# Kernel tuning notes

Hardware: AMD Instinct MI355X
Metric: run time of the kernel (lower is better)

The kernel has to match this reference:

```python
import jax, jax.numpy as jnp
import numpy as np

ITERS = 10
SMOOTH = 1e-06


def _pool(x, wh, ww, ph, pw, is_max):
    # torch max_pool2d pads with -inf; min-pool (=-maxpool(-x)) thus pads with +inf.
    init = -jnp.inf if is_max else jnp.inf
    op = jax.lax.max if is_max else jax.lax.min
    return jax.lax.reduce_window(
        x, init, op,
        window_dimensions=(1, 1, wh, ww),
        window_strides=(1, 1, 1, 1),
        padding=((0, 0), (0, 0), (ph, ph), (pw, pw)))


def soft_erode(img):
    p1 = _pool(img, 3, 1, 1, 0, is_max=False)  # min over 3x1 window
    p2 = _pool(img, 1, 3, 0, 1, is_max=False)  # min over 1x3 window
    return jnp.minimum(p1, p2)


def soft_dilate(img):
    return _pool(img, 3, 3, 1, 1, is_max=True)


def soft_open(img):
    return soft_dilate(soft_erode(img))


def soft_skel(img, iters=ITERS):
    skel = jnp.zeros_like(img)
    for _ in range(iters):  # fixed small trip count; unrolled under jit
        opened = soft_open(img)
        skel = skel + jax.nn.relu(img - opened)
        img = soft_erode(img)
    return skel


def setup_inputs() -> dict:
    key = jax.random.key(0)
    k1, k2 = jax.random.split(key)
    B, C, H, W = 16, 1, 512, 512
    pred = jax.random.normal(k1, (B, C, H, W), dtype=jnp.float32)  # logits
    target = jax.random.randint(k2, (B, C, H, W), 0, 2).astype(jnp.float32)
    return {"pred": pred, "target": target}


def reference(pred, target):
    p = jax.nn.sigmoid(pred)
    skel_pred = soft_skel(p, ITERS)
    skel_gt = soft_skel(target.astype(jnp.float32), ITERS)
    tprec = jnp.sum(p * skel_gt) / (jnp.sum(skel_gt) + SMOOTH)
    tsens = jnp.sum(target * skel_pred) / (jnp.sum(skel_pred) + SMOOTH)
    cldice = 2.0 * tprec * tsens / (tprec + tsens + SMOOTH)
    return 1.0 - cldice
```

## Files before the change

kernel.cpp:

```cpp
#include <hip/hip_runtime.h>
#include <math.h>

#define HH 512
#define WW 512
#define NBATCH 16
#define RV 16
#define FSV (HH/RV)
#define FSH 5
#define NF (NBATCH*FSH*FSV)
#define BSU 13
#define BSV 4
#define NBT (NBATCH*BSU*BSV)
#define NTASK (NF + NBT)
#define FINF  (__builtin_huge_valf())

typedef _Float16 h2 __attribute__((ext_vector_type(2)));

__device__ __forceinline__ float sigf(float x) { return 1.0f / (1.0f + __expf(-x)); }
__device__ __forceinline__ unsigned bpermu(int a, unsigned v) {
    return (unsigned)__builtin_amdgcn_ds_bpermute(a, (int)v);
}
__device__ __forceinline__ h2 h2bits(unsigned u) { return __builtin_bit_cast(h2, u); }
__device__ __forceinline__ unsigned bitsh2(h2 h) { return __builtin_bit_cast(unsigned, h); }
__device__ __forceinline__ h2 hmin2(h2 a, h2 b) { return __builtin_elementwise_min(a, b); }
__device__ __forceinline__ h2 hmax2(h2 a, h2 b) { return __builtin_elementwise_max(a, b); }
__device__ __forceinline__ h2 dpp_prev(h2 v) {
    unsigned u = bitsh2(v);
    return h2bits((unsigned)__builtin_amdgcn_update_dpp((int)u, (int)u, 0x130, 0xF, 0xF, false));
}
__device__ __forceinline__ h2 dpp_next(h2 v) {
    unsigned u = bitsh2(v);
    return h2bits((unsigned)__builtin_amdgcn_update_dpp((int)u, (int)u, 0x138, 0xF, 0xF, false));
}
#if __has_builtin(__builtin_amdgcn_alignbit)
__device__ __forceinline__ h2 lvec2(h2 prev, h2 self) {
    return h2bits(__builtin_amdgcn_alignbit(bitsh2(self), bitsh2(prev), 16));
}
__device__ __forceinline__ h2 rvec2(h2 self, h2 next) {
    return h2bits(__builtin_amdgcn_alignbit(bitsh2(next), bitsh2(self), 16));
}
#else
__device__ __forceinline__ h2 lvec2(h2 prev, h2 self) {
    return h2bits((bitsh2(prev) >> 16) | (bitsh2(self) << 16));
}
__device__ __forceinline__ h2 rvec2(h2 self, h2 next) {
    return h2bits((bitsh2(self) >> 16) | (bitsh2(next) << 16));
}
#endif

template<bool GUARD>
__device__ __forceinline__ void do_strip(
    const float* __restrict__ ip, const float* __restrict__ wp,
    int r0, bool ok0, bool ok1, bool useX, bool useY,
    h2 eclamp, h2 dclamp,
    float* __restrict__ partials, int wid, int lane)
{
    const h2 HP = h2bits(0x7C007C00u);
    const h2 HN = h2bits(0xFC00FC00u);
    const h2 HZ = h2bits(0u);

    h2 W[11][3], sk[10];
#pragma unroll
    for (int t = 0; t < 11; ++t) { W[t][0] = HP; W[t][1] = HP; W[t][2] = HP; }
#pragma unroll
    for (int j = 0; j < 10; ++j) sk[j] = HZ;
    float wsx = 0.f, wsy = 0.f, rsx = 0.f, rsy = 0.f;

#define LOADROW(fv)                                                     \
    h2 nv;                                                              \
    {                                                                   \
        if (!GUARD || (unsigned)(fv) < (unsigned)HH) {                  \
            float2 t0 = *(const float2*)(ip);                           \
            float x = sigf(t0.x); x = ok0 ? x : FINF;                   \
            float y = sigf(t0.y); y = ok1 ? y : FINF;                   \
            nv[0] = (_Float16)x; nv[1] = (_Float16)y;                   \
        } else nv = HP;                                                 \
        ip += WW;                                                       \
    }

#define ALEVEL(t)                                                       \
    {                                                                   \
        W[t][0] = W[t][1]; W[t][1] = W[t][2]; W[t][2] = nr;             \
        h2 a0 = W[t][0], a1 = W[t][1], a2 = W[t][2];                    \
        h2 vmin = hmin2(hmin2(a0, a1), a2);                             \
        h2 pv = dpp_prev(a1), nx = dpp_next(a1);                        \
        h2 lv = lvec2(pv, a1), rv = rvec2(a1, nx);                      \
        h2 e = hmin2(vmin, hmin2(lv, rv));                              \
        nr = hmax2(e, eclamp);                                          \
    }

#define BLEVEL(t, fv)                                                   \
    {                                                                   \
        h2 b0 = W[t+1][0], b1 = W[t+1][1], b2 = W[t+1][2];              \
        if (GUARD) {                                                    \
            if ((unsigned)((fv) - t - 4) >= (unsigned)HH) b0 = HN;      \
            if ((unsigned)((fv) - t - 3) >= (unsigned)HH) b1 = HN;      \
            if ((unsigned)((fv) - t - 2) >= (unsigned)HH) b2 = HN;      \
        }                                                               \
        h2 cm = hmin2(hmax2(hmax2(b0, b1), b2), dclamp);                \
        h2 pv = dpp_prev(cm), nx = dpp_next(cm);                        \
        h2 lv = lvec2(pv, cm), rv = rvec2(cm, nx);                      \
        h2 d = hmax2(cm, hmax2(lv, rv));                                \
        h2 df = hmax2(W[t][0] - d, HZ);                                 \
        if (t == 0) sk[9] = df; else sk[9-t] = sk[9-t] + df;            \
    }

#define RINGSHIFT()                                                     \
    {                                                                   \
        _Pragma("unroll")                                               \
        for (int j = 0; j < 9; ++j) sk[j] = sk[j + 1];                  \
    }

#define FINAL()                                                         \
    {                                                                   \
        float2 wv = *(const float2*)(wp); wp += WW;                     \
        float c0v = (float)sk[0][0];                                    \
        float c1v = (float)sk[0][1];                                    \
        float cx = useX ? c0v : 0.f;                                    \
        float cy = useY ? c1v : 0.f;                                    \
        wsx += wv.x * cx; wsy += wv.y * cy;                             \
        rsx += cx;        rsy += cy;                                    \
    }

    for (int s = 0; s < 14; ++s) {
        const int f = r0 - 11 + s;
        LOADROW(f);
        h2 nr = nv;
#pragma unroll
        for (int t = 0; t < 6; ++t) {
            if (s >= 2 * t) ALEVEL(t);
        }
        W[6][0] = W[6][1]; W[6][1] = W[6][2]; W[6][2] = nr;
    }
    for (int s = 14; s < 23; ++s) {
        const int f = r0 - 11 + s;
        LOADROW(f);
        RINGSHIFT();
#pragma unroll
        for (int t = 0; t < 10; ++t) {
            if (t <= s - 14) BLEVEL(t, f);
        }
        h2 nr = nv;
#pragma unroll
        for (int t = 0; t < 10; ++t) ALEVEL(t);
        W[10][0] = W[10][1]; W[10][1] = W[10][2]; W[10][2] = nr;
    }
    for (int s = 23; s < 38; ++s) {
        const int f = r0 - 11 + s;
        LOADROW(f);
        RINGSHIFT();
#pragma unroll
        for (int t = 0; t < 10; ++t) BLEVEL(t, f);
        FINAL();
        h2 nr = nv;
#pragma unroll
        for (int t = 0; t < 10; ++t) ALEVEL(t);
        W[10][0] = W[10][1]; W[10][1] = W[10][2]; W[10][2] = nr;
    }
    {
        const int f = r0 - 11 + 38;
        RINGSHIFT();
#pragma unroll
        for (int t = 0; t < 10; ++t) BLEVEL(t, f);
        FINAL();
    }

#undef LOADROW
#undef ALEVEL
#undef BLEVEL
#undef RINGSHIFT
#undef FINAL

    float pw = wsx + wsy;
    float pr = rsx + rsy;
#pragma unroll
    for (int off = 32; off; off >>= 1) {
        pw += __shfl_down(pw, off, 64);
        pr += __shfl_down(pr, off, 64);
    }
    if (lane == 0) { partials[2 * wid] = pw; partials[2 * wid + 1] = pr; }
}

__device__ void do_bits(const float* __restrict__ tgt, const float* __restrict__ prd,
                        int b, int u, int v, float* __restrict__ partials,
                        int wid, int lane)
{
    const int c = u * 40 - 12 + lane;
    const bool inImg = (c >= 0) && (c < WW);
    const int cc = min(max(c, 0), WW - 1);
    const size_t base = (size_t)b * HH * WW;
    const int w0 = 4 * v - 1;
    const int aL = ((lane + 63) & 63) << 2;
    const int aR = ((lane + 1) & 63) << 2;
    const bool vtop = (v == 0), vbot = (v == BSV - 1);

    unsigned w[6];
#pragma unroll
    for (int k = 0; k < 6; ++k) {
        const int gw = w0 + k;
        unsigned acc = 0xFFFFFFFFu;
        if (gw >= 0 && gw < 16) {
            acc = 0u;
            const float* rp = tgt + base + (size_t)(gw * 32) * WW + cc;
            for (int i = 0; i < 32; ++i) {
                acc |= ((__float_as_uint(*rp) >> 29) & 1u) << i;
                rp += WW;
            }
            acc = inImg ? acc : 0xFFFFFFFFu;
        }
        w[k] = acc;
    }

    unsigned P0[4] = {0,0,0,0}, P1[4] = {0,0,0,0}, P2[4] = {0,0,0,0}, P3[4] = {0,0,0,0};

#pragma unroll
    for (int t = 0; t < 10; ++t) {
        unsigned E[6];
#pragma unroll
        for (int k = 0; k < 6; ++k) {
            unsigned up = (w[k] << 1) | (k > 0 ? (w[k-1] >> 31) : 1u);
            unsigned dn = (w[k] >> 1) | (k < 5 ? (w[k+1] << 31) : 0x80000000u);
            unsigned vert = w[k] & up & dn;
            unsigned Lw = bpermu(aL, w[k]);
            unsigned Rw = bpermu(aR, w[k]);
            unsigned e = vert & Lw & Rw;
            E[k] = inImg ? e : 0xFFFFFFFFu;
        }
        if (vtop) E[0] = 0xFFFFFFFFu;
        if (vbot) E[5] = 0xFFFFFFFFu;

        const unsigned t0 = vtop ? 0u : E[0];
        const unsigned t5 = vbot ? 0u : E[5];
#pragma unroll
        for (int k = 1; k <= 4; ++k) {
            unsigned eu = (k == 1) ? t0 : E[k-1];
            unsigned ed = (k == 4) ? t5 : E[k+1];
            unsigned up = (E[k] << 1) | (eu >> 31);
            unsigned dn = (E[k] >> 1) | (ed << 31);
            unsigned V  = E[k] | up | dn;
            unsigned Vm = inImg ? V : 0u;
            unsigned D  = Vm | bpermu(aL, Vm) | bpermu(aR, Vm);
            unsigned contrib = w[k] & ~D;
            unsigned c0 = contrib & P0[k-1];  P0[k-1] ^= contrib;
            unsigned c1 = c0 & P1[k-1];       P1[k-1] ^= c0;
            unsigned c2 = c1 & P2[k-1];       P2[k-1] ^= c1;
            P3[k-1] ^= c2;
        }
#pragma unroll
        for (int k = 0; k < 6; ++k) w[k] = E[k];
    }

    const bool useful = inImg && (lane >= 12) && (lane < 52);
    unsigned rsum = 0;
#pragma unroll
    for (int k = 0; k < 4; ++k) {
        if (!useful) { P0[k] = 0; P1[k] = 0; P2[k] = 0; P3[k] = 0; }
        rsum += __popc(P0[k]) + 2*__popc(P1[k]) + 4*__popc(P2[k]) + 8*__popc(P3[k]);
    }
    float wsum = 0.f;
    const float* pp = prd + base + (size_t)(128 * v) * WW + cc;
    for (int i = 0; i < 32; ++i) {
#pragma unroll
        for (int k = 0; k < 4; ++k) {
            unsigned cnt = ((P0[k] >> i) & 1u) + (((P1[k] >> i) & 1u) << 1)
                         + (((P2[k] >> i) & 1u) << 2) + (((P3[k] >> i) & 1u) << 3);
            float p = sigf(pp[(size_t)(32 * k + i) * WW]);
            wsum += p * (float)cnt;
        }
    }

    float pw = wsum, pr = (float)rsum;
#pragma unroll
    for (int off = 32; off; off >>= 1) {
        pw += __shfl_down(pw, off, 64);
        pr += __shfl_down(pr, off, 64);
    }
    if (lane == 0) { partials[2 * wid] = pw; partials[2 * wid + 1] = pr; }
}

__global__ __launch_bounds__(64)
void cld_main(const float* __restrict__ pred, const float* __restrict__ target,
              float* __restrict__ partials)
{
    const int wid  = blockIdx.x;
    const int lane = threadIdx.x;

    if (wid < NF) {
        int t_ = wid;
        const int b = t_ / (FSH * FSV);  t_ -= b * (FSH * FSV);
        const int u = t_ / FSV;
        const int v = t_ - u * FSV;
        const int r0 = v * RV;
        const int cbase = u * 102 - 12;
        const int UW = (u == FSH - 1) ? 104 : 102;

        const int c0 = cbase + 2 * lane;
        const int c1 = c0 + 1;
        const bool ok0 = (c0 >= 0) && (c0 < WW);
        const bool ok1 = (c1 >= 0) && (c1 < WW);
        const int wc0 = 2 * lane;
        const bool useX = (wc0     >= 12) && (wc0     < 12 + UW);
        const bool useY = (wc0 + 1 >= 12) && (wc0 + 1 < 12 + UW);
        const unsigned elo = ok0 ? 0xFC00u : 0x7C00u;
        const unsigned ehi = ok1 ? 0xFC00u : 0x7C00u;
        const h2 eclamp = h2bits(elo | (ehi << 16));
        const h2 dclamp = h2bits((elo | (ehi << 16)) ^ 0x80008000u);
        const int cc = min(max(c0, 0), WW - 2);

        const float* ip = pred   + (size_t)b * HH * WW + (ptrdiff_t)(r0 - 11) * WW + cc;
        const float* wp = target + (size_t)b * HH * WW + (size_t)r0 * WW + cc;

        if (v == 0 || v == FSV - 1)
            do_strip<true >(ip, wp, r0, ok0, ok1, useX, useY, eclamp, dclamp, partials, wid, lane);
        else
            do_strip<false>(ip, wp, r0, ok0, ok1, useX, useY, eclamp, dclamp, partials, wid, lane);
    } else {
        int idx = wid - NF;
        const int b = idx / (BSU * BSV);  idx -= b * (BSU * BSV);
        const int u = idx / BSV;
        const int v = idx - u * BSV;
        do_bits(target, pred, b, u, v, partials, wid, lane);
    }
}

__global__ void cld_final(const float* __restrict__ partials, float* __restrict__ out)
{
    const int tid = threadIdx.x;
    double a0 = 0, a1 = 0, a2 = 0, a3 = 0;
    for (int i = tid; i < NF; i += 256) {
        a0 += (double)partials[2 * i];
        a1 += (double)partials[2 * i + 1];
    }
    for (int i = NF + tid; i < NTASK; i += 256) {
        a2 += (double)partials[2 * i];
        a3 += (double)partials[2 * i + 1];
    }
    __shared__ double red[256][4];
    red[tid][0] = a0; red[tid][1] = a1; red[tid][2] = a2; red[tid][3] = a3;
    __syncthreads();
    for (int s2 = 128; s2 > 0; s2 >>= 1) {
        if (tid < s2) {
            red[tid][0] += red[tid + s2][0]; red[tid][1] += red[tid + s2][1];
            red[tid][2] += red[tid + s2][2]; red[tid][3] += red[tid + s2][3];
        }
        __syncthreads();
    }
    if (tid == 0) {
        double tsens = red[0][0] / (red[0][1] + 1e-6);
        double tprec = red[0][2] / (red[0][3] + 1e-6);
        double cl = 2.0 * tprec * tsens / (tprec + tsens + 1e-6);
        out[0] = (float)(1.0 - cl);
    }
}

extern "C" void kernel_launch(void* const* d_in, const int* in_sizes, int n_in,
                              void* d_out, int out_size, void* d_ws, size_t ws_size,
                              hipStream_t stream) {
    const float* pred   = (const float*)d_in[0];
    const float* target = (const float*)d_in[1];
    float* out = (float*)d_out;
    float* partials = (float*)d_ws;

    hipLaunchKernelGGL(cld_main, dim3(NTASK), dim3(64), 0, stream,
                       pred, target, partials);
    hipLaunchKernelGGL(cld_final, dim3(1), dim3(256), 0, stream, partials, out);
}
```

Before: 73.57 us.

## Double strip height and software-prefetch next input and weight rows

Raises rows per strip from 16 to 32, which halves the number of strip tasks and amortizes the 22-row halo warm-up over more output rows. The row loads are restructured so the next input row and the next weight row are fetched one iteration ahead of their use, hiding global load latency behind the erode/dilate ALU work. The trade-off is fewer tasks to spread across the GPU, longer serial strips and a few more live registers.

Result: slower. 79.60 us (+8.2%).

```diff
diff --git a/kernel.cpp b/kernel.cpp
--- a/kernel.cpp
+++ b/kernel.cpp
@@ -4,7 +4,7 @@
 #define HH 512
 #define WW 512
 #define NBATCH 16
-#define RV 16
+#define RV 32
 #define FSV (HH/RV)
 #define FSH 5
 #define NF (NBATCH*FSH*FSV)
@@ -12,6 +12,7 @@
 #define BSV 4
 #define NBT (NBATCH*BSU*BSV)
 #define NTASK (NF + NBT)
+#define NSTEP (RV + 23)
 #define FINF  (__builtin_huge_valf())
 
 typedef _Float16 h2 __attribute__((ext_vector_type(2)));
@@ -66,15 +67,26 @@
     for (int j = 0; j < 10; ++j) sk[j] = HZ;
     float wsx = 0.f, wsy = 0.f, rsx = 0.f, rsy = 0.f;
 
-#define LOADROW(fv)                                                     \
+    float2 raw;
+    if (!GUARD || (unsigned)(r0 - 11) < (unsigned)HH) raw = *(const float2*)ip;
+    ip += WW;
+    float2 wnext = *(const float2*)wp;
+    wp += WW;
+
+#define CVTROW(fv)                                                      \
     h2 nv;                                                              \
     {                                                                   \
         if (!GUARD || (unsigned)(fv) < (unsigned)HH) {                  \
-            float2 t0 = *(const float2*)(ip);                           \
-            float x = sigf(t0.x); x = ok0 ? x : FINF;                   \
-            float y = sigf(t0.y); y = ok1 ? y : FINF;                   \
+            float x = sigf(raw.x); x = ok0 ? x : FINF;                  \
+            float y = sigf(raw.y); y = ok1 ? y : FINF;                  \
             nv[0] = (_Float16)x; nv[1] = (_Float16)y;                   \
         } else nv = HP;                                                 \
+    }
+
+#define PREFETCH(fnext)                                                 \
+    {                                                                   \
+        if (!GUARD || (unsigned)(fnext) < (unsigned)HH)                 \
+            raw = *(const float2*)ip;                                   \
         ip += WW;                                                       \
     }
 
@@ -111,20 +123,20 @@
         for (int j = 0; j < 9; ++j) sk[j] = sk[j + 1];                  \
     }
 
-#define FINAL()                                                         \
-    {                                                                   \
-        float2 wv = *(const float2*)(wp); wp += WW;                     \
+#define FINAL(wv)                                                       \
+    {                                                                   \
         float c0v = (float)sk[0][0];                                    \
         float c1v = (float)sk[0][1];                                    \
         float cx = useX ? c0v : 0.f;                                    \
         float cy = useY ? c1v : 0.f;                                    \
-        wsx += wv.x * cx; wsy += wv.y * cy;                             \
-        rsx += cx;        rsy += cy;                                    \
+        wsx += (wv).x * cx; wsy += (wv).y * cy;                         \
+        rsx += cx;          rsy += cy;                                  \
     }
 
     for (int s = 0; s < 14; ++s) {
         const int f = r0 - 11 + s;
-        LOADROW(f);
+        CVTROW(f);
+        PREFETCH(f + 1);
         h2 nr = nv;
 #pragma unroll
         for (int t = 0; t < 6; ++t) {
@@ -134,7 +146,8 @@
     }
     for (int s = 14; s < 23; ++s) {
         const int f = r0 - 11 + s;
-        LOADROW(f);
+        CVTROW(f);
+        PREFETCH(f + 1);
         RINGSHIFT();
 #pragma unroll
         for (int t = 0; t < 10; ++t) {
@@ -145,27 +158,31 @@
         for (int t = 0; t < 10; ++t) ALEVEL(t);
         W[10][0] = W[10][1]; W[10][1] = W[10][2]; W[10][2] = nr;
     }
-    for (int s = 23; s < 38; ++s) {
+    for (int s = 23; s < NSTEP - 1; ++s) {
         const int f = r0 - 11 + s;
-        LOADROW(f);
+        CVTROW(f);
+        if (s < NSTEP - 2) PREFETCH(f + 1);
+        float2 wcur = wnext;
+        if (s < NSTEP - 2) { wnext = *(const float2*)wp; wp += WW; }
         RINGSHIFT();
 #pragma unroll
         for (int t = 0; t < 10; ++t) BLEVEL(t, f);
-        FINAL();
+        FINAL(wcur);
         h2 nr = nv;
 #pragma unroll
         for (int t = 0; t < 10; ++t) ALEVEL(t);
         W[10][0] = W[10][1]; W[10][1] = W[10][2]; W[10][2] = nr;
     }
     {
-        const int f = r0 - 11 + 38;
+        const int f = r0 - 11 + NSTEP - 1;
         RINGSHIFT();
 #pragma unroll
         for (int t = 0; t < 10; ++t) BLEVEL(t, f);
-        FINAL();
-    }
-
-#undef LOADROW
+        FINAL(wnext);
+    }
+
+#undef CVTROW
+#undef PREFETCH
 #undef ALEVEL
 #undef BLEVEL
 #undef RINGSHIFT
```
